# Performance work log

Measured on AMD Instinct MI355X. Metric: run time of the kernel, lower is better.

Reference implementation:

```python
import jax, jax.numpy as jnp
import numpy as np

E, D, H, N = 16, 1024, 4096, 16384  # experts, idim, hidden_units, total tokens


def setup_inputs() -> dict:
    key = jax.random.key(0)
    k1, k2, k3, k4, k5 = jax.random.split(key, 5)
    s1 = 1.0 / np.sqrt(D)  # kaiming-uniform-ish bound for fan_in=D
    s2 = 1.0 / np.sqrt(H)
    return {
        "xs": jax.random.normal(k1, (N, D), dtype=jnp.float32),
        # tokens are grouped contiguously per expert; uniform load here
        "fwd_expert_count": jnp.full((E,), N // E, dtype=jnp.int32),
        "w1": jax.random.uniform(k2, (E, H, D), jnp.float32, -s1, s1),
        "b1": jax.random.uniform(k3, (E, H), jnp.float32, -s1, s1),
        "w2": jax.random.uniform(k4, (E, D, H), jnp.float32, -s2, s2),
        "b2": jax.random.uniform(k5, (E, D), jnp.float32, -s2, s2),
    }


def reference(xs, fwd_expert_count, w1, b1, w2, b2):
    # Grouped GEMM expert FFN (FMoELinear -> ReLU -> FMoELinear).
    # Counts are uniform (N//E per expert), so the per-expert grouped GEMM
    # is exactly a batched matmul over the expert axis.
    x = xs.reshape(E, N // E, D)                       # [E, n, D]
    h = jnp.einsum('end,ehd->enh', x, w1) + b1[:, None, :]  # [E, n, H]
    h = jax.nn.relu(h)                                 # dropout_rate=0 -> identity
    y = jnp.einsum('enh,edh->end', h, w2) + b2[:, None, :]  # [E, n, D]
    return y.reshape(N, D)
```

## Files before the change

kernel.cpp:

```cpp
#include <hip/hip_runtime.h>

#define E_  16
#define D_  1024
#define H_  4096
#define NPE 1024

typedef __bf16 bf16x8 __attribute__((ext_vector_type(8)));
typedef float f32x4 __attribute__((ext_vector_type(4)));

__device__ __forceinline__ unsigned short f2bf(float f) {
  unsigned int u = __float_as_uint(f);
  u += 0x7fffu + ((u >> 16) & 1u);
  return (unsigned short)(u >> 16);
}

__global__ __launch_bounds__(256) void cvt_f32_to_bf16(
    const float* __restrict__ in, unsigned short* __restrict__ out, int nvec) {
  int i = blockIdx.x * 256 + threadIdx.x;
  if (i >= nvec) return;
  float4 v = ((const float4*)in)[i];
  ushort4 o;
  o.x = f2bf(v.x);
  o.y = f2bf(v.y);
  o.z = f2bf(v.z);
  o.w = f2bf(v.w);
  ((ushort4*)out)[i] = o;
}

template <bool RELU_BF16_OUT>
__global__ __launch_bounds__(256) void gemm_bt(
    const unsigned short* __restrict__ A,
    const unsigned short* __restrict__ B,
    const float* __restrict__ bias,
    void* __restrict__ Cout,
    int M, int N, int K) {
  __shared__ unsigned short ldsA[128 * 32];
  __shared__ unsigned short ldsB[128 * 32];

  const int tid  = threadIdx.x;
  const int lane = tid & 63;
  const int wave = tid >> 6;
  const int wm   = wave >> 1;
  const int wn   = wave & 1;
  const int fr   = lane & 15;
  const int fq   = lane >> 4;

  const int Mt = M >> 7;
  const int Nt = N >> 7;
  const int id     = blockIdx.x;
  const int region = id & 7;
  const int slot   = id >> 3;
  const int bpe    = Mt * Nt;
  const int eloc   = slot / bpe;
  const int rem    = slot - eloc * bpe;
  const int e      = region * (E_ / 8) + eloc;
  const int SN     = Nt < 8 ? Nt : 8;
  const int csz    = Mt * SN;
  const int chunk  = rem / csz;
  const int inner  = rem - chunk * csz;
  const int mt     = inner % Mt;
  const int nt     = chunk * SN + inner / Mt;

  const int bm = mt << 7;
  const int bn = nt << 7;

  const unsigned short* Ae = A + (size_t)e * M * K;
  const unsigned short* Be = B + (size_t)e * N * K;

  const int srow = tid >> 2;
  const int qp   = tid & 3;
  const int qg   = qp ^ ((srow >> 1) & 3);

  const size_t arow0 = (size_t)(bm + srow) * K + qg * 8;
  const size_t arow1 = (size_t)(bm + srow + 64) * K + qg * 8;
  const size_t brow0 = (size_t)(bn + srow) * K + qg * 8;
  const size_t brow1 = (size_t)(bn + srow + 64) * K + qg * 8;
  unsigned short* lA0 = ldsA + wave * 512;
  unsigned short* lA1 = ldsA + 2048 + wave * 512;
  unsigned short* lB0 = ldsB + wave * 512;
  unsigned short* lB1 = ldsB + 2048 + wave * 512;

  f32x4 acc[4][4];
  const f32x4 zero = {0.f, 0.f, 0.f, 0.f};
#pragma unroll
  for (int i = 0; i < 4; ++i)
#pragma unroll
    for (int j = 0; j < 4; ++j) acc[i][j] = zero;

  int aoff[4], boff[4];
#pragma unroll
  for (int i = 0; i < 4; ++i) {
    int ra = wm * 64 + i * 16 + fr;
    aoff[i] = ra * 32 + ((fq ^ ((ra >> 1) & 3)) << 3);
    int rb = wn * 64 + i * 16 + fr;
    boff[i] = rb * 32 + ((fq ^ ((rb >> 1) & 3)) << 3);
  }

  const int kIters = K >> 5;
  for (int kt = 0; kt < kIters; ++kt) {
    const int k0 = kt << 5;
    __syncthreads();
    __builtin_amdgcn_global_load_lds((const unsigned int*)(Ae + arow0 + k0),
                                     (unsigned int*)lA0, 16, 0, 0);
    __builtin_amdgcn_global_load_lds((const unsigned int*)(Ae + arow1 + k0),
                                     (unsigned int*)lA1, 16, 0, 0);
    __builtin_amdgcn_global_load_lds((const unsigned int*)(Be + brow0 + k0),
                                     (unsigned int*)lB0, 16, 0, 0);
    __builtin_amdgcn_global_load_lds((const unsigned int*)(Be + brow1 + k0),
                                     (unsigned int*)lB1, 16, 0, 0);
    __syncthreads();

    bf16x8 af[4], bfr[4];
#pragma unroll
    for (int i = 0; i < 4; ++i) af[i] = *(const bf16x8*)&ldsA[aoff[i]];
#pragma unroll
    for (int i = 0; i < 4; ++i) bfr[i] = *(const bf16x8*)&ldsB[boff[i]];

#pragma unroll
    for (int mi = 0; mi < 4; ++mi)
#pragma unroll
      for (int ni = 0; ni < 4; ++ni)
        acc[mi][ni] = __builtin_amdgcn_mfma_f32_16x16x32_bf16(af[mi], bfr[ni],
                                                              acc[mi][ni], 0, 0, 0);
  }

  const int crow0 = bm + wm * 64 + fq * 4;
  const int ccol0 = bn + wn * 64 + fr;
  float bv[4];
#pragma unroll
  for (int ni = 0; ni < 4; ++ni) bv[ni] = bias[(size_t)e * N + ccol0 + ni * 16];

  if (RELU_BF16_OUT) {
    unsigned short* C = (unsigned short*)Cout + (size_t)e * M * N;
#pragma unroll
    for (int mi = 0; mi < 4; ++mi)
#pragma unroll
      for (int ni = 0; ni < 4; ++ni)
#pragma unroll
        for (int r = 0; r < 4; ++r) {
          float v = acc[mi][ni][r] + bv[ni];
          v = v > 0.f ? v : 0.f;
          C[(size_t)(crow0 + mi * 16 + r) * N + ccol0 + ni * 16] = f2bf(v);
        }
  } else {
    float* C = (float*)Cout + (size_t)e * M * N;
#pragma unroll
    for (int mi = 0; mi < 4; ++mi)
#pragma unroll
      for (int ni = 0; ni < 4; ++ni)
#pragma unroll
        for (int r = 0; r < 4; ++r) {
          C[(size_t)(crow0 + mi * 16 + r) * N + ccol0 + ni * 16] =
              acc[mi][ni][r] + bv[ni];
        }
  }
}

extern "C" void kernel_launch(void* const* d_in, const int* in_sizes, int n_in,
                              void* d_out, int out_size, void* d_ws, size_t ws_size,
                              hipStream_t stream) {
  (void)in_sizes; (void)n_in; (void)out_size; (void)ws_size;
  const float* xs = (const float*)d_in[0];
  const float* w1 = (const float*)d_in[2];
  const float* b1 = (const float*)d_in[3];
  const float* w2 = (const float*)d_in[4];
  const float* b2 = (const float*)d_in[5];
  float* y = (float*)d_out;

  char* ws = (char*)d_ws;
  unsigned short* xs_bf = (unsigned short*)ws;
  unsigned short* w_bf  = (unsigned short*)(ws + (size_t)(32u << 20));
  unsigned short* h_bf  = (unsigned short*)(ws + (size_t)(160u << 20));

  const int nXs = E_ * NPE * D_;
  const int nW  = E_ * H_ * D_;

  cvt_f32_to_bf16<<<nXs / 4 / 256, 256, 0, stream>>>(xs, xs_bf, nXs / 4);
  cvt_f32_to_bf16<<<nW / 4 / 256, 256, 0, stream>>>(w1, w_bf, nW / 4);

  gemm_bt<true><<<E_ * (NPE / 128) * (H_ / 128), 256, 0, stream>>>(
      xs_bf, w_bf, b1, h_bf, NPE, H_, D_);

  cvt_f32_to_bf16<<<nW / 4 / 256, 256, 0, stream>>>(w2, w_bf, nW / 4);

  gemm_bt<false><<<E_ * (NPE / 128) * (D_ / 128), 256, 0, stream>>>(
      h_bf, w_bf, b2, y, NPE, D_, H_);
}
```

Measured before the change: 1.035 ms.

## Use 256x256 tiles with 512 threads and 4-stage async LDS pipeline

The GEMM moves from 128x128 tiles with 256 threads and a single LDS buffer to 256x256 tiles with 8 waves, each computing 128x64. Global-to-LDS loads run three stages ahead in a four-deep ring buffer with explicit vmcnt waits, and MFMA blocks are wrapped in setprio. This is meant to hide global memory latency and raise data reuse per tile. The costs are 128KB of LDS per block, more accumulator registers, and fewer blocks for the second GEMM (256 blocks), which may underfill the GPU.

```diff
diff --git a/kernel.cpp b/kernel.cpp
--- a/kernel.cpp
+++ b/kernel.cpp
@@ -27,26 +27,32 @@
   ((ushort4*)out)[i] = o;
 }
 
+__device__ __forceinline__ void wg_barrier() {
+  asm volatile("" ::: "memory");
+  __builtin_amdgcn_s_barrier();
+  asm volatile("" ::: "memory");
+}
+
 template <bool RELU_BF16_OUT>
-__global__ __launch_bounds__(256) void gemm_bt(
+__global__ __launch_bounds__(512, 2) void gemm_bt(
     const unsigned short* __restrict__ A,
     const unsigned short* __restrict__ B,
     const float* __restrict__ bias,
     void* __restrict__ Cout,
     int M, int N, int K) {
-  __shared__ unsigned short ldsA[128 * 32];
-  __shared__ unsigned short ldsB[128 * 32];
+  __shared__ __attribute__((aligned(16))) unsigned short ldsA[4 * 256 * 32];
+  __shared__ __attribute__((aligned(16))) unsigned short ldsB[4 * 256 * 32];
 
   const int tid  = threadIdx.x;
   const int lane = tid & 63;
   const int wave = tid >> 6;
-  const int wm   = wave >> 1;
-  const int wn   = wave & 1;
+  const int wm   = wave >> 2;
+  const int wn   = wave & 3;
   const int fr   = lane & 15;
   const int fq   = lane >> 4;
 
-  const int Mt = M >> 7;
-  const int Nt = N >> 7;
+  const int Mt = M >> 8;
+  const int Nt = N >> 8;
   const int id     = blockIdx.x;
   const int region = id & 7;
   const int slot   = id >> 3;
@@ -54,77 +60,100 @@
   const int eloc   = slot / bpe;
   const int rem    = slot - eloc * bpe;
   const int e      = region * (E_ / 8) + eloc;
-  const int SN     = Nt < 8 ? Nt : 8;
+  const int SN     = Nt < 2 ? Nt : 2;
   const int csz    = Mt * SN;
   const int chunk  = rem / csz;
   const int inner  = rem - chunk * csz;
   const int mt     = inner % Mt;
   const int nt     = chunk * SN + inner / Mt;
 
-  const int bm = mt << 7;
-  const int bn = nt << 7;
+  const int bm = mt << 8;
+  const int bn = nt << 8;
 
   const unsigned short* Ae = A + (size_t)e * M * K;
   const unsigned short* Be = B + (size_t)e * N * K;
 
-  const int srow = tid >> 2;
-  const int qp   = tid & 3;
-  const int qg   = qp ^ ((srow >> 1) & 3);
-
-  const size_t arow0 = (size_t)(bm + srow) * K + qg * 8;
-  const size_t arow1 = (size_t)(bm + srow + 64) * K + qg * 8;
-  const size_t brow0 = (size_t)(bn + srow) * K + qg * 8;
-  const size_t brow1 = (size_t)(bn + srow + 64) * K + qg * 8;
-  unsigned short* lA0 = ldsA + wave * 512;
-  unsigned short* lA1 = ldsA + 2048 + wave * 512;
-  unsigned short* lB0 = ldsB + wave * 512;
-  unsigned short* lB1 = ldsB + 2048 + wave * 512;
-
-  f32x4 acc[4][4];
+  const int srow   = lane >> 2;
+  const int schunk = (lane & 3) ^ ((lane >> 3) & 3);
+  const size_t aSrc0 = (size_t)(bm + wave * 16 + srow) * K + schunk * 8;
+  const size_t aSrc1 = (size_t)(bm + 128 + wave * 16 + srow) * K + schunk * 8;
+  const size_t bSrc0 = (size_t)(bn + wave * 16 + srow) * K + schunk * 8;
+  const size_t bSrc1 = (size_t)(bn + 128 + wave * 16 + srow) * K + schunk * 8;
+
+#define STAGE(KT)                                                              \
+  do {                                                                         \
+    const int _bo = ((KT) & 3) * 8192 + wave * 512;                            \
+    const size_t _k = (size_t)(KT) << 5;                                       \
+    __builtin_amdgcn_global_load_lds((const unsigned int*)(Ae + aSrc0 + _k),   \
+                                     (unsigned int*)(ldsA + _bo), 16, 0, 0);   \
+    __builtin_amdgcn_global_load_lds((const unsigned int*)(Ae + aSrc1 + _k),   \
+                                     (unsigned int*)(ldsA + _bo + 4096), 16, 0, 0); \
+    __builtin_amdgcn_global_load_lds((const unsigned int*)(Be + bSrc0 + _k),   \
+                                     (unsigned int*)(ldsB + _bo), 16, 0, 0);   \
+    __builtin_amdgcn_global_load_lds((const unsigned int*)(Be + bSrc1 + _k),   \
+                                     (unsigned int*)(ldsB + _bo + 4096), 16, 0, 0); \
+  } while (0)
+
+  const int swz   = (fq ^ ((fr >> 1) & 3)) << 3;
+  const int abase = (wm * 128 + fr) * 32 + swz;
+  const int bbase = (wn * 64 + fr) * 32 + swz;
+
+  f32x4 acc[8][4];
   const f32x4 zero = {0.f, 0.f, 0.f, 0.f};
 #pragma unroll
-  for (int i = 0; i < 4; ++i)
+  for (int i = 0; i < 8; ++i)
 #pragma unroll
     for (int j = 0; j < 4; ++j) acc[i][j] = zero;
 
-  int aoff[4], boff[4];
-#pragma unroll
-  for (int i = 0; i < 4; ++i) {
-    int ra = wm * 64 + i * 16 + fr;
-    aoff[i] = ra * 32 + ((fq ^ ((ra >> 1) & 3)) << 3);
-    int rb = wn * 64 + i * 16 + fr;
-    boff[i] = rb * 32 + ((fq ^ ((rb >> 1) & 3)) << 3);
+  const int nK = K >> 5;
+  STAGE(0);
+  if (nK > 1) STAGE(1);
+  if (nK > 2) STAGE(2);
+
+#pragma unroll 1
+  for (int kt = 0; kt < nK; ++kt) {
+    if (kt + 3 < nK) STAGE(kt + 3);
+    asm volatile("s_waitcnt vmcnt(12)" ::: "memory");
+    wg_barrier();
+
+    const unsigned short* lA = ldsA + (kt & 3) * 8192;
+    const unsigned short* lB = ldsB + (kt & 3) * 8192;
+
+    bf16x8 af[4], bfr[4];
+#pragma unroll
+    for (int i = 0; i < 4; ++i) af[i] = *(const bf16x8*)&lA[abase + i * 512];
+#pragma unroll
+    for (int i = 0; i < 4; ++i) bfr[i] = *(const bf16x8*)&lB[bbase + i * 512];
+
+    wg_barrier();
+    asm volatile("s_waitcnt lgkmcnt(0)" ::: "memory");
+    __builtin_amdgcn_s_setprio(1);
+#pragma unroll
+    for (int mi = 0; mi < 4; ++mi)
+#pragma unroll
+      for (int ni = 0; ni < 4; ++ni)
+        acc[mi][ni] = __builtin_amdgcn_mfma_f32_16x16x32_bf16(
+            af[mi], bfr[ni], acc[mi][ni], 0, 0, 0);
+    __builtin_amdgcn_s_setprio(0);
+    wg_barrier();
+
+#pragma unroll
+    for (int i = 0; i < 4; ++i)
+      af[i] = *(const bf16x8*)&lA[abase + 2048 + i * 512];
+    asm volatile("s_waitcnt lgkmcnt(0)" ::: "memory");
+    __builtin_amdgcn_s_setprio(1);
+#pragma unroll
+    for (int mi = 0; mi < 4; ++mi)
+#pragma unroll
+      for (int ni = 0; ni < 4; ++ni)
+        acc[4 + mi][ni] = __builtin_amdgcn_mfma_f32_16x16x32_bf16(
+            af[mi], bfr[ni], acc[4 + mi][ni], 0, 0, 0);
+    __builtin_amdgcn_s_setprio(0);
+    wg_barrier();
   }
-
-  const int kIters = K >> 5;
-  for (int kt = 0; kt < kIters; ++kt) {
-    const int k0 = kt << 5;
-    __syncthreads();
-    __builtin_amdgcn_global_load_lds((const unsigned int*)(Ae + arow0 + k0),
-                                     (unsigned int*)lA0, 16, 0, 0);
-    __builtin_amdgcn_global_load_lds((const unsigned int*)(Ae + arow1 + k0),
-                                     (unsigned int*)lA1, 16, 0, 0);
-    __builtin_amdgcn_global_load_lds((const unsigned int*)(Be + brow0 + k0),
-                                     (unsigned int*)lB0, 16, 0, 0);
-    __builtin_amdgcn_global_load_lds((const unsigned int*)(Be + brow1 + k0),
-                                     (unsigned int*)lB1, 16, 0, 0);
-    __syncthreads();
-
-    bf16x8 af[4], bfr[4];
-#pragma unroll
-    for (int i = 0; i < 4; ++i) af[i] = *(const bf16x8*)&ldsA[aoff[i]];
-#pragma unroll
-    for (int i = 0; i < 4; ++i) bfr[i] = *(const bf16x8*)&ldsB[boff[i]];
-
-#pragma unroll
-    for (int mi = 0; mi < 4; ++mi)
-#pragma unroll
-      for (int ni = 0; ni < 4; ++ni)
-        acc[mi][ni] = __builtin_amdgcn_mfma_f32_16x16x32_bf16(af[mi], bfr[ni],
-                                                              acc[mi][ni], 0, 0, 0);
-  }
-
-  const int crow0 = bm + wm * 64 + fq * 4;
+#undef STAGE
+
+  const int crow0 = bm + wm * 128 + fq * 4;
   const int ccol0 = bn + wn * 64 + fr;
   float bv[4];
 #pragma unroll
@@ -133,7 +162,7 @@
   if (RELU_BF16_OUT) {
     unsigned short* C = (unsigned short*)Cout + (size_t)e * M * N;
 #pragma unroll
-    for (int mi = 0; mi < 4; ++mi)
+    for (int mi = 0; mi < 8; ++mi)
 #pragma unroll
       for (int ni = 0; ni < 4; ++ni)
 #pragma unroll
@@ -145,7 +174,7 @@
   } else {
     float* C = (float*)Cout + (size_t)e * M * N;
 #pragma unroll
-    for (int mi = 0; mi < 4; ++mi)
+    for (int mi = 0; mi < 8; ++mi)
 #pragma unroll
       for (int ni = 0; ni < 4; ++ni)
 #pragma unroll
@@ -178,11 +207,11 @@
   cvt_f32_to_bf16<<<nXs / 4 / 256, 256, 0, stream>>>(xs, xs_bf, nXs / 4);
   cvt_f32_to_bf16<<<nW / 4 / 256, 256, 0, stream>>>(w1, w_bf, nW / 4);
 
-  gemm_bt<true><<<E_ * (NPE / 128) * (H_ / 128), 256, 0, stream>>>(
+  gemm_bt<true><<<E_ * (NPE / 256) * (H_ / 256), 512, 0, stream>>>(
       xs_bf, w_bf, b1, h_bf, NPE, H_, D_);
 
   cvt_f32_to_bf16<<<nW / 4 / 256, 256, 0, stream>>>(w2, w_bf, nW / 4);
 
-  gemm_bt<false><<<E_ * (NPE / 128) * (D_ / 128), 256, 0, stream>>>(
+  gemm_bt<false><<<E_ * (NPE / 256) * (D_ / 256), 512, 0, stream>>>(
       h_bf, w_bf, b2, y, NPE, D_, H_);
 }
```

Result: faster. 995.4 us (-3.8%).
